# Optimization experiments

Hardware: AMD Instinct MI355X
Metric: run time of the kernel (lower is better)

The kernel has to match this reference:

```python
import jax, jax.numpy as jnp
from jax import lax
import numpy as np

B, M, N, NUM_ITER = 8192, 256, 512, 16


def setup_inputs() -> dict:
    key = jax.random.key(0)
    k1, k2, k3, k4, k5 = jax.random.split(key, 5)
    y = jax.random.normal(k1, (B, M), dtype=jnp.float32)
    # Scale S/D/W so the unrolled recurrence stays numerically stable over 16 steps
    S = jax.random.normal(k2, (N, N), dtype=jnp.float32) * (0.9 / np.sqrt(N))
    W = jax.random.normal(k3, (N, M), dtype=jnp.float32) * (0.1 / np.sqrt(M))
    D = jax.random.normal(k4, (N, N), dtype=jnp.float32) * (1.0 / np.sqrt(N))
    thr = jax.random.uniform(k5, (1, 1), dtype=jnp.float32) * 0.1
    return {"y": y, "S": S, "W": W, "D": D, "thr": thr, "numIter": NUM_ITER}


def soft_thr(u, theta):
    return jax.nn.relu(u - theta) - jax.nn.relu(-u - theta)


def reference(y, S, W, D, thr, numIter):
    # Batch-first rewrite of: d = (D.T @ soft_thr(D @ (S@d.T + W@y.T), thr)).T
    Wy = y @ W.T  # (B, N), invariant across iterations
    d0 = jnp.zeros((y.shape[0], S.shape[0]), dtype=y.dtype)

    def step(d, _):
        z = d @ S.T + Wy          # (B, N)
        u = z @ D.T               # (B, N)  == (D @ z.T).T
        d_new = soft_thr(u, thr) @ D  # (B, N) == (D.T @ s.T).T
        return d_new, d_new

    _, ds = lax.scan(step, d0, None, length=numIter)
    # Original returns list [d0, d1, ..., d_numIter]; stack as one array
    return jnp.concatenate([d0[None], ds], axis=0)  # (numIter+1, B, N)
```

## Files before the change

kernel.cpp:

```cpp
#include <hip/hip_runtime.h>

#define B_SZ 8192
#define M_SZ 256
#define N_SZ 512
#define TB 64
#define THREADS 1024
#define LDP 520
#define LDPY 264
#define NITER 16

typedef _Float16 half8 __attribute__((ext_vector_type(8)));
typedef _Float16 half4 __attribute__((ext_vector_type(4)));
typedef float floatx4 __attribute__((ext_vector_type(4)));

__global__ void conv_kernel(const float* __restrict__ W, const float* __restrict__ D,
                            _Float16* __restrict__ Wf, _Float16* __restrict__ Df,
                            _Float16* __restrict__ Dtf) {
  int i = blockIdx.x * blockDim.x + threadIdx.x;
  if (i < N_SZ * N_SZ) {
    float d = D[i];
    Df[i] = (_Float16)d;
    int r = i >> 9;
    int c = i & (N_SZ - 1);
    Dtf[c * N_SZ + r] = (_Float16)d;
  }
  if (i < N_SZ * M_SZ) Wf[i] = (_Float16)W[i];
}

__global__ __launch_bounds__(256) void ecomp_kernel(const float* __restrict__ S,
                                                    const float* __restrict__ D,
                                                    _Float16* __restrict__ Ef) {
  __shared__ float Dst[8 * N_SZ];
  const int tid = threadIdx.x;
  const int r0 = blockIdx.x * 8;
  for (int i = tid; i < 8 * N_SZ; i += 256) Dst[i] = D[(size_t)r0 * N_SZ + i];
  __syncthreads();
  float acc[8][2];
#pragma unroll
  for (int r = 0; r < 8; ++r) acc[r][0] = acc[r][1] = 0.f;
#pragma unroll 4
  for (int j = 0; j < N_SZ; ++j) {
    float s0 = S[(size_t)j * N_SZ + tid];
    float s1 = S[(size_t)j * N_SZ + tid + 256];
#pragma unroll
    for (int r = 0; r < 8; ++r) {
      float dv = Dst[r * N_SZ + j];
      acc[r][0] += dv * s0;
      acc[r][1] += dv * s1;
    }
  }
#pragma unroll
  for (int r = 0; r < 8; ++r) {
    Ef[(size_t)(r0 + r) * N_SZ + tid] = (_Float16)acc[r][0];
    Ef[(size_t)(r0 + r) * N_SZ + tid + 256] = (_Float16)acc[r][1];
  }
}

__global__ __launch_bounds__(THREADS) void ista_kernel(
    const float* __restrict__ y, const _Float16* __restrict__ Ef,
    const _Float16* __restrict__ Df, const _Float16* __restrict__ Dtf,
    const _Float16* __restrict__ Wf, const float* __restrict__ thrp,
    float* __restrict__ out) {
  __shared__ _Float16 bufA[TB * LDP];
  __shared__ _Float16 bufB[TB * LDP];

  const int tid = threadIdx.x;
  const int wave = tid >> 6;
  const int lane = tid & 63;
  const int m16 = lane & 15;
  const int q = lane >> 4;
  const int rowBase = blockIdx.x * TB;
  const int colBase = wave * 32;

  {
    const int r = tid >> 4;
    const int c0 = (tid & 15) << 4;
    const float* src = y + (size_t)(rowBase + r) * M_SZ + c0;
#pragma unroll
    for (int j = 0; j < 16; j += 4) {
      float4 v = *reinterpret_cast<const float4*>(src + j);
      _Float16* dst = &bufA[r * LDPY + c0 + j];
      dst[0] = (_Float16)v.x;
      dst[1] = (_Float16)v.y;
      dst[2] = (_Float16)v.z;
      dst[3] = (_Float16)v.w;
    }
  }
  __syncthreads();

  floatx4 acc[4][2];

#pragma unroll
  for (int rt = 0; rt < 4; ++rt) acc[rt][0] = acc[rt][1] = (floatx4){0.f, 0.f, 0.f, 0.f};
#pragma unroll 2
  for (int ks = 0; ks < M_SZ / 32; ++ks) {
    half8 a0 = *reinterpret_cast<const half8*>(&bufA[m16 * LDPY + ks * 32 + q * 8]);
    half8 a1 = *reinterpret_cast<const half8*>(&bufA[(16 + m16) * LDPY + ks * 32 + q * 8]);
    half8 a2 = *reinterpret_cast<const half8*>(&bufA[(32 + m16) * LDPY + ks * 32 + q * 8]);
    half8 a3 = *reinterpret_cast<const half8*>(&bufA[(48 + m16) * LDPY + ks * 32 + q * 8]);
#pragma unroll
    for (int ct = 0; ct < 2; ++ct) {
      half8 b = *reinterpret_cast<const half8*>(Wf + (size_t)(colBase + ct * 16 + m16) * M_SZ + ks * 32 + q * 8);
      acc[0][ct] = __builtin_amdgcn_mfma_f32_16x16x32_f16(a0, b, acc[0][ct], 0, 0, 0);
      acc[1][ct] = __builtin_amdgcn_mfma_f32_16x16x32_f16(a1, b, acc[1][ct], 0, 0, 0);
      acc[2][ct] = __builtin_amdgcn_mfma_f32_16x16x32_f16(a2, b, acc[2][ct], 0, 0, 0);
      acc[3][ct] = __builtin_amdgcn_mfma_f32_16x16x32_f16(a3, b, acc[3][ct], 0, 0, 0);
    }
  }
#pragma unroll
  for (int rt = 0; rt < 4; ++rt)
#pragma unroll
    for (int ct = 0; ct < 2; ++ct)
#pragma unroll
      for (int r = 0; r < 4; ++r)
        bufB[(rt * 16 + q * 4 + r) * LDP + colBase + ct * 16 + m16] = (_Float16)acc[rt][ct][r];
  __syncthreads();

  auto gemmK512 = [&](const _Float16* Abuf, const _Float16* __restrict__ Bmat) {
    const _Float16* arow = Abuf + m16 * LDP + q * 8;
    const _Float16* brow0 = Bmat + (size_t)(colBase + m16) * N_SZ + q * 8;
    const _Float16* brow1 = Bmat + (size_t)(colBase + 16 + m16) * N_SZ + q * 8;
#pragma unroll 2
    for (int ks = 0; ks < N_SZ / 32; ++ks) {
      half8 a0 = *reinterpret_cast<const half8*>(arow + ks * 32);
      half8 a1 = *reinterpret_cast<const half8*>(arow + 16 * LDP + ks * 32);
      half8 a2 = *reinterpret_cast<const half8*>(arow + 32 * LDP + ks * 32);
      half8 a3 = *reinterpret_cast<const half8*>(arow + 48 * LDP + ks * 32);
      half8 b0 = *reinterpret_cast<const half8*>(brow0 + ks * 32);
      half8 b1 = *reinterpret_cast<const half8*>(brow1 + ks * 32);
      acc[0][0] = __builtin_amdgcn_mfma_f32_16x16x32_f16(a0, b0, acc[0][0], 0, 0, 0);
      acc[0][1] = __builtin_amdgcn_mfma_f32_16x16x32_f16(a0, b1, acc[0][1], 0, 0, 0);
      acc[1][0] = __builtin_amdgcn_mfma_f32_16x16x32_f16(a1, b0, acc[1][0], 0, 0, 0);
      acc[1][1] = __builtin_amdgcn_mfma_f32_16x16x32_f16(a1, b1, acc[1][1], 0, 0, 0);
      acc[2][0] = __builtin_amdgcn_mfma_f32_16x16x32_f16(a2, b0, acc[2][0], 0, 0, 0);
      acc[2][1] = __builtin_amdgcn_mfma_f32_16x16x32_f16(a2, b1, acc[2][1], 0, 0, 0);
      acc[3][0] = __builtin_amdgcn_mfma_f32_16x16x32_f16(a3, b0, acc[3][0], 0, 0, 0);
      acc[3][1] = __builtin_amdgcn_mfma_f32_16x16x32_f16(a3, b1, acc[3][1], 0, 0, 0);
    }
  };

#pragma unroll
  for (int rt = 0; rt < 4; ++rt) acc[rt][0] = acc[rt][1] = (floatx4){0.f, 0.f, 0.f, 0.f};
  gemmK512(bufB, Df);
  half4 ch[4][2];
#pragma unroll
  for (int rt = 0; rt < 4; ++rt)
#pragma unroll
    for (int ct = 0; ct < 2; ++ct)
#pragma unroll
      for (int r = 0; r < 4; ++r) ch[rt][ct][r] = (_Float16)acc[rt][ct][r];

  {
    int* za = reinterpret_cast<int*>(bufA);
    for (int i = tid; i < TB * LDP / 2; i += THREADS) za[i] = 0;
    float4 z4 = {0.f, 0.f, 0.f, 0.f};
    float4* o4 = reinterpret_cast<float4*>(out + (size_t)rowBase * N_SZ);
    for (int i = tid; i < TB * N_SZ / 4; i += THREADS) o4[i] = z4;
  }
  __syncthreads();

  const float thrv = *thrp;

#pragma unroll 1
  for (int it = 1; it <= NITER; ++it) {
#pragma unroll
    for (int rt = 0; rt < 4; ++rt) acc[rt][0] = acc[rt][1] = (floatx4){0.f, 0.f, 0.f, 0.f};
    gemmK512(bufA, Ef);
#pragma unroll
    for (int rt = 0; rt < 4; ++rt)
#pragma unroll
      for (int ct = 0; ct < 2; ++ct)
#pragma unroll
        for (int r = 0; r < 4; ++r) {
          float u = acc[rt][ct][r] + (float)ch[rt][ct][r];
          float s = fmaxf(u - thrv, 0.f) - fmaxf(-u - thrv, 0.f);
          bufB[(rt * 16 + q * 4 + r) * LDP + colBase + ct * 16 + m16] = (_Float16)s;
        }
    __syncthreads();

#pragma unroll
    for (int rt = 0; rt < 4; ++rt) acc[rt][0] = acc[rt][1] = (floatx4){0.f, 0.f, 0.f, 0.f};
    gemmK512(bufB, Dtf);
#pragma unroll
    for (int rt = 0; rt < 4; ++rt)
#pragma unroll
      for (int ct = 0; ct < 2; ++ct)
#pragma unroll
        for (int r = 0; r < 4; ++r)
          bufA[(rt * 16 + q * 4 + r) * LDP + colBase + ct * 16 + m16] = (_Float16)acc[rt][ct][r];
    __syncthreads();

    float* oslice = out + ((size_t)it * B_SZ + rowBase) * N_SZ;
#pragma unroll
    for (int i = tid; i < TB * N_SZ / 8; i += THREADS) {
      int r = i >> 6;
      int c8 = (i & 63) << 3;
      half8 h = *reinterpret_cast<const half8*>(&bufA[r * LDP + c8]);
      float4 lo = {(float)h[0], (float)h[1], (float)h[2], (float)h[3]};
      float4 hi = {(float)h[4], (float)h[5], (float)h[6], (float)h[7]};
      float* dst = oslice + (size_t)r * N_SZ + c8;
      *reinterpret_cast<float4*>(dst) = lo;
      *reinterpret_cast<float4*>(dst + 4) = hi;
    }
  }
}

extern "C" void kernel_launch(void* const* d_in, const int* in_sizes, int n_in,
                              void* d_out, int out_size, void* d_ws, size_t ws_size,
                              hipStream_t stream) {
  const float* y = (const float*)d_in[0];
  const float* S = (const float*)d_in[1];
  const float* W = (const float*)d_in[2];
  const float* D = (const float*)d_in[3];
  const float* thr = (const float*)d_in[4];
  float* out = (float*)d_out;

  char* ws = (char*)d_ws;
  _Float16* Ef = (_Float16*)(ws);
  _Float16* Df = (_Float16*)(ws + 512 * 1024);
  _Float16* Dtf = (_Float16*)(ws + 1024 * 1024);
  _Float16* Wf = (_Float16*)(ws + 1536 * 1024);

  conv_kernel<<<(N_SZ * N_SZ + 255) / 256, 256, 0, stream>>>(W, D, Wf, Df, Dtf);
  ecomp_kernel<<<N_SZ / 8, 256, 0, stream>>>(S, D, Ef);
  ista_kernel<<<B_SZ / TB, THREADS, 0, stream>>>(y, Ef, Df, Dtf, Wf, thr, out);
}
```

Measured before the change: 845.4 us.

## Use MFMA for E precompute, swap GEMM operands, prefetch weights, store output directly

The scalar fp32 E=D*S precompute becomes an MFMA kernel fed by fp16 copies of D and a transposed S written in the conversion kernel. In the ISTA kernel the MFMA operands are swapped so each lane's accumulator rows map to contiguous columns, which allows half4 LDS stores and float4 global stores. Weight fragments are prefetched PF steps ahead in registers. The output slice is written straight from the accumulators rather than re-read from LDS after a sync, which also writes fp32 values instead of values rounded through fp16. Launch bounds now request 4 blocks, which adds register pressure.

Measured after the change: 883.0 us. 1.04x slower.

```diff
diff --git a/kernel.cpp b/kernel.cpp
--- a/kernel.cpp
+++ b/kernel.cpp
@@ -8,55 +8,68 @@
 #define LDP 520
 #define LDPY 264
 #define NITER 16
+#define PF 4
 
 typedef _Float16 half8 __attribute__((ext_vector_type(8)));
 typedef _Float16 half4 __attribute__((ext_vector_type(4)));
 typedef float floatx4 __attribute__((ext_vector_type(4)));
 
-__global__ void conv_kernel(const float* __restrict__ W, const float* __restrict__ D,
+__global__ void conv_kernel(const float* __restrict__ S, const float* __restrict__ W,
+                            const float* __restrict__ D,
                             _Float16* __restrict__ Wf, _Float16* __restrict__ Df,
-                            _Float16* __restrict__ Dtf) {
+                            _Float16* __restrict__ Dtf, _Float16* __restrict__ Stf) {
   int i = blockIdx.x * blockDim.x + threadIdx.x;
   if (i < N_SZ * N_SZ) {
+    int r = i >> 9;
+    int c = i & (N_SZ - 1);
     float d = D[i];
     Df[i] = (_Float16)d;
-    int r = i >> 9;
-    int c = i & (N_SZ - 1);
     Dtf[c * N_SZ + r] = (_Float16)d;
+    Stf[c * N_SZ + r] = (_Float16)S[i];
   }
   if (i < N_SZ * M_SZ) Wf[i] = (_Float16)W[i];
 }
 
-__global__ __launch_bounds__(256) void ecomp_kernel(const float* __restrict__ S,
-                                                    const float* __restrict__ D,
+__global__ __launch_bounds__(256) void ecomp_kernel(const _Float16* __restrict__ Df,
+                                                    const _Float16* __restrict__ Stf,
                                                     _Float16* __restrict__ Ef) {
-  __shared__ float Dst[8 * N_SZ];
   const int tid = threadIdx.x;
-  const int r0 = blockIdx.x * 8;
-  for (int i = tid; i < 8 * N_SZ; i += 256) Dst[i] = D[(size_t)r0 * N_SZ + i];
-  __syncthreads();
-  float acc[8][2];
-#pragma unroll
-  for (int r = 0; r < 8; ++r) acc[r][0] = acc[r][1] = 0.f;
-#pragma unroll 4
-  for (int j = 0; j < N_SZ; ++j) {
-    float s0 = S[(size_t)j * N_SZ + tid];
-    float s1 = S[(size_t)j * N_SZ + tid + 256];
-#pragma unroll
-    for (int r = 0; r < 8; ++r) {
-      float dv = Dst[r * N_SZ + j];
-      acc[r][0] += dv * s0;
-      acc[r][1] += dv * s1;
-    }
-  }
-#pragma unroll
-  for (int r = 0; r < 8; ++r) {
-    Ef[(size_t)(r0 + r) * N_SZ + tid] = (_Float16)acc[r][0];
-    Ef[(size_t)(r0 + r) * N_SZ + tid + 256] = (_Float16)acc[r][1];
-  }
-}
-
-__global__ __launch_bounds__(THREADS) void ista_kernel(
+  const int wave = tid >> 6;
+  const int lane = tid & 63;
+  const int m16 = lane & 15;
+  const int q = lane >> 4;
+  const int i0 = (blockIdx.x & 7) * 64;
+  const int j0 = (blockIdx.x >> 3) * 128 + wave * 32;
+
+  floatx4 acc[4][2];
+#pragma unroll
+  for (int it = 0; it < 4; ++it) acc[it][0] = acc[it][1] = (floatx4){0.f, 0.f, 0.f, 0.f};
+
+  const _Float16* dp = Df + (size_t)(i0 + m16) * N_SZ + q * 8;
+  const _Float16* sp = Stf + (size_t)(j0 + m16) * N_SZ + q * 8;
+#pragma unroll
+  for (int ks = 0; ks < N_SZ / 32; ++ks) {
+    half8 s0 = *reinterpret_cast<const half8*>(sp + ks * 32);
+    half8 s1 = *reinterpret_cast<const half8*>(sp + 16 * N_SZ + ks * 32);
+#pragma unroll
+    for (int it = 0; it < 4; ++it) {
+      half8 dv = *reinterpret_cast<const half8*>(dp + (size_t)it * 16 * N_SZ + ks * 32);
+      acc[it][0] = __builtin_amdgcn_mfma_f32_16x16x32_f16(s0, dv, acc[it][0], 0, 0, 0);
+      acc[it][1] = __builtin_amdgcn_mfma_f32_16x16x32_f16(s1, dv, acc[it][1], 0, 0, 0);
+    }
+  }
+#pragma unroll
+  for (int it = 0; it < 4; ++it)
+#pragma unroll
+    for (int jt = 0; jt < 2; ++jt) {
+      half4 h;
+#pragma unroll
+      for (int r = 0; r < 4; ++r) h[r] = (_Float16)acc[it][jt][r];
+      *reinterpret_cast<half4*>(Ef + (size_t)(i0 + it * 16 + m16) * N_SZ + j0 + jt * 16 + q * 4) = h;
+    }
+}
+
+__global__ __launch_bounds__(THREADS, 4) void ista_kernel(
     const float* __restrict__ y, const _Float16* __restrict__ Ef,
     const _Float16* __restrict__ Df, const _Float16* __restrict__ Dtf,
     const _Float16* __restrict__ Wf, const float* __restrict__ thrp,
@@ -92,56 +105,63 @@
 
 #pragma unroll
   for (int rt = 0; rt < 4; ++rt) acc[rt][0] = acc[rt][1] = (floatx4){0.f, 0.f, 0.f, 0.f};
-#pragma unroll 2
-  for (int ks = 0; ks < M_SZ / 32; ++ks) {
-    half8 a0 = *reinterpret_cast<const half8*>(&bufA[m16 * LDPY + ks * 32 + q * 8]);
-    half8 a1 = *reinterpret_cast<const half8*>(&bufA[(16 + m16) * LDPY + ks * 32 + q * 8]);
-    half8 a2 = *reinterpret_cast<const half8*>(&bufA[(32 + m16) * LDPY + ks * 32 + q * 8]);
-    half8 a3 = *reinterpret_cast<const half8*>(&bufA[(48 + m16) * LDPY + ks * 32 + q * 8]);
+  {
+    const _Float16* yp = bufA + m16 * LDPY + q * 8;
+    const _Float16* wp0 = Wf + (size_t)(colBase + m16) * M_SZ + q * 8;
+    const _Float16* wp1 = wp0 + 16 * M_SZ;
+#pragma unroll
+    for (int ks = 0; ks < M_SZ / 32; ++ks) {
+      half8 b0 = *reinterpret_cast<const half8*>(wp0 + ks * 32);
+      half8 b1 = *reinterpret_cast<const half8*>(wp1 + ks * 32);
+#pragma unroll
+      for (int rt = 0; rt < 4; ++rt) {
+        half8 a = *reinterpret_cast<const half8*>(yp + rt * 16 * LDPY + ks * 32);
+        acc[rt][0] = __builtin_amdgcn_mfma_f32_16x16x32_f16(b0, a, acc[rt][0], 0, 0, 0);
+        acc[rt][1] = __builtin_amdgcn_mfma_f32_16x16x32_f16(b1, a, acc[rt][1], 0, 0, 0);
+      }
+    }
+  }
+#pragma unroll
+  for (int rt = 0; rt < 4; ++rt)
 #pragma unroll
     for (int ct = 0; ct < 2; ++ct) {
-      half8 b = *reinterpret_cast<const half8*>(Wf + (size_t)(colBase + ct * 16 + m16) * M_SZ + ks * 32 + q * 8);
-      acc[0][ct] = __builtin_amdgcn_mfma_f32_16x16x32_f16(a0, b, acc[0][ct], 0, 0, 0);
-      acc[1][ct] = __builtin_amdgcn_mfma_f32_16x16x32_f16(a1, b, acc[1][ct], 0, 0, 0);
-      acc[2][ct] = __builtin_amdgcn_mfma_f32_16x16x32_f16(a2, b, acc[2][ct], 0, 0, 0);
-      acc[3][ct] = __builtin_amdgcn_mfma_f32_16x16x32_f16(a3, b, acc[3][ct], 0, 0, 0);
-    }
-  }
-#pragma unroll
-  for (int rt = 0; rt < 4; ++rt)
-#pragma unroll
-    for (int ct = 0; ct < 2; ++ct)
-#pragma unroll
-      for (int r = 0; r < 4; ++r)
-        bufB[(rt * 16 + q * 4 + r) * LDP + colBase + ct * 16 + m16] = (_Float16)acc[rt][ct][r];
+      half4 h;
+#pragma unroll
+      for (int r = 0; r < 4; ++r) h[r] = (_Float16)acc[rt][ct][r];
+      *reinterpret_cast<half4*>(&bufB[(rt * 16 + m16) * LDP + colBase + ct * 16 + q * 4]) = h;
+    }
   __syncthreads();
 
-  auto gemmK512 = [&](const _Float16* Abuf, const _Float16* __restrict__ Bmat) {
-    const _Float16* arow = Abuf + m16 * LDP + q * 8;
-    const _Float16* brow0 = Bmat + (size_t)(colBase + m16) * N_SZ + q * 8;
-    const _Float16* brow1 = Bmat + (size_t)(colBase + 16 + m16) * N_SZ + q * 8;
-#pragma unroll 2
+  auto gemmK512T = [&](const _Float16* Xbuf, const _Float16* __restrict__ Bmat) {
+    const _Float16* xp = Xbuf + m16 * LDP + q * 8;
+    const _Float16* bp0 = Bmat + (size_t)(colBase + m16) * N_SZ + q * 8;
+    const _Float16* bp1 = bp0 + 16 * N_SZ;
+    half8 mp[PF][2];
+#pragma unroll
+    for (int p = 0; p < PF; ++p) {
+      mp[p][0] = *reinterpret_cast<const half8*>(bp0 + p * 32);
+      mp[p][1] = *reinterpret_cast<const half8*>(bp1 + p * 32);
+    }
+#pragma unroll
     for (int ks = 0; ks < N_SZ / 32; ++ks) {
-      half8 a0 = *reinterpret_cast<const half8*>(arow + ks * 32);
-      half8 a1 = *reinterpret_cast<const half8*>(arow + 16 * LDP + ks * 32);
-      half8 a2 = *reinterpret_cast<const half8*>(arow + 32 * LDP + ks * 32);
-      half8 a3 = *reinterpret_cast<const half8*>(arow + 48 * LDP + ks * 32);
-      half8 b0 = *reinterpret_cast<const half8*>(brow0 + ks * 32);
-      half8 b1 = *reinterpret_cast<const half8*>(brow1 + ks * 32);
-      acc[0][0] = __builtin_amdgcn_mfma_f32_16x16x32_f16(a0, b0, acc[0][0], 0, 0, 0);
-      acc[0][1] = __builtin_amdgcn_mfma_f32_16x16x32_f16(a0, b1, acc[0][1], 0, 0, 0);
-      acc[1][0] = __builtin_amdgcn_mfma_f32_16x16x32_f16(a1, b0, acc[1][0], 0, 0, 0);
-      acc[1][1] = __builtin_amdgcn_mfma_f32_16x16x32_f16(a1, b1, acc[1][1], 0, 0, 0);
-      acc[2][0] = __builtin_amdgcn_mfma_f32_16x16x32_f16(a2, b0, acc[2][0], 0, 0, 0);
-      acc[2][1] = __builtin_amdgcn_mfma_f32_16x16x32_f16(a2, b1, acc[2][1], 0, 0, 0);
-      acc[3][0] = __builtin_amdgcn_mfma_f32_16x16x32_f16(a3, b0, acc[3][0], 0, 0, 0);
-      acc[3][1] = __builtin_amdgcn_mfma_f32_16x16x32_f16(a3, b1, acc[3][1], 0, 0, 0);
+      half8 b0 = mp[ks % PF][0];
+      half8 b1 = mp[ks % PF][1];
+      if (ks + PF < N_SZ / 32) {
+        mp[ks % PF][0] = *reinterpret_cast<const half8*>(bp0 + (ks + PF) * 32);
+        mp[ks % PF][1] = *reinterpret_cast<const half8*>(bp1 + (ks + PF) * 32);
+      }
+#pragma unroll
+      for (int xt = 0; xt < 4; ++xt) {
+        half8 a = *reinterpret_cast<const half8*>(xp + xt * 16 * LDP + ks * 32);
+        acc[xt][0] = __builtin_amdgcn_mfma_f32_16x16x32_f16(b0, a, acc[xt][0], 0, 0, 0);
+        acc[xt][1] = __builtin_amdgcn_mfma_f32_16x16x32_f16(b1, a, acc[xt][1], 0, 0, 0);
+      }
     }
   };
 
 #pragma unroll
   for (int rt = 0; rt < 4; ++rt) acc[rt][0] = acc[rt][1] = (floatx4){0.f, 0.f, 0.f, 0.f};
-  gemmK512(bufB, Df);
+  gemmK512T(bufB, Df);
   half4 ch[4][2];
 #pragma unroll
   for (int rt = 0; rt < 4; ++rt)
@@ -165,43 +185,42 @@
   for (int it = 1; it <= NITER; ++it) {
 #pragma unroll
     for (int rt = 0; rt < 4; ++rt) acc[rt][0] = acc[rt][1] = (floatx4){0.f, 0.f, 0.f, 0.f};
-    gemmK512(bufA, Ef);
+    gemmK512T(bufA, Ef);
 #pragma unroll
     for (int rt = 0; rt < 4; ++rt)
 #pragma unroll
-      for (int ct = 0; ct < 2; ++ct)
+      for (int ct = 0; ct < 2; ++ct) {
+        half4 h;
 #pragma unroll
         for (int r = 0; r < 4; ++r) {
           float u = acc[rt][ct][r] + (float)ch[rt][ct][r];
           float s = fmaxf(u - thrv, 0.f) - fmaxf(-u - thrv, 0.f);
-          bufB[(rt * 16 + q * 4 + r) * LDP + colBase + ct * 16 + m16] = (_Float16)s;
+          h[r] = (_Float16)s;
         }
+        *reinterpret_cast<half4*>(&bufB[(rt * 16 + m16) * LDP + colBase + ct * 16 + q * 4]) = h;
+      }
     __syncthreads();
 
 #pragma unroll
     for (int rt = 0; rt < 4; ++rt) acc[rt][0] = acc[rt][1] = (floatx4){0.f, 0.f, 0.f, 0.f};
-    gemmK512(bufB, Dtf);
+    gemmK512T(bufB, Dtf);
+    float* oslice = out + ((size_t)it * B_SZ + rowBase) * N_SZ;
 #pragma unroll
     for (int rt = 0; rt < 4; ++rt)
 #pragma unroll
-      for (int ct = 0; ct < 2; ++ct)
-#pragma unroll
-        for (int r = 0; r < 4; ++r)
-          bufA[(rt * 16 + q * 4 + r) * LDP + colBase + ct * 16 + m16] = (_Float16)acc[rt][ct][r];
+      for (int ct = 0; ct < 2; ++ct) {
+        half4 h;
+        float4 f;
+#pragma unroll
+        for (int r = 0; r < 4; ++r) {
+          float v = acc[rt][ct][r];
+          h[r] = (_Float16)v;
+          reinterpret_cast<float*>(&f)[r] = v;
+        }
+        *reinterpret_cast<half4*>(&bufA[(rt * 16 + m16) * LDP + colBase + ct * 16 + q * 4]) = h;
+        *reinterpret_cast<float4*>(oslice + (size_t)(rt * 16 + m16) * N_SZ + colBase + ct * 16 + q * 4) = f;
+      }
     __syncthreads();
-
-    float* oslice = out + ((size_t)it * B_SZ + rowBase) * N_SZ;
-#pragma unroll
-    for (int i = tid; i < TB * N_SZ / 8; i += THREADS) {
-      int r = i >> 6;
-      int c8 = (i & 63) << 3;
-      half8 h = *reinterpret_cast<const half8*>(&bufA[r * LDP + c8]);
-      float4 lo = {(float)h[0], (float)h[1], (float)h[2], (float)h[3]};
-      float4 hi = {(float)h[4], (float)h[5], (float)h[6], (float)h[7]};
-      float* dst = oslice + (size_t)r * N_SZ + c8;
-      *reinterpret_cast<float4*>(dst) = lo;
-      *reinterpret_cast<float4*>(dst + 4) = hi;
-    }
   }
 }
 
@@ -220,8 +239,9 @@
   _Float16* Df = (_Float16*)(ws + 512 * 1024);
   _Float16* Dtf = (_Float16*)(ws + 1024 * 1024);
   _Float16* Wf = (_Float16*)(ws + 1536 * 1024);
-
-  conv_kernel<<<(N_SZ * N_SZ + 255) / 256, 256, 0, stream>>>(W, D, Wf, Df, Dtf);
-  ecomp_kernel<<<N_SZ / 8, 256, 0, stream>>>(S, D, Ef);
+  _Float16* Stf = (_Float16*)(ws + 1792 * 1024);
+
+  conv_kernel<<<(N_SZ * N_SZ + 255) / 256, 256, 0, stream>>>(S, W, D, Wf, Df, Dtf, Stf);
+  ecomp_kernel<<<32, 256, 0, stream>>>(Df, Stf, Ef);
   ista_kernel<<<B_SZ / TB, THREADS, 0, stream>>>(y, Ef, Df, Dtf, Wf, thr, out);
 }
```
